# Optimization experiments

Measured on AMD Instinct MI355X. Metric: run time of the kernel, lower is better.

## Reference

```python
import jax, jax.numpy as jnp
import numpy as np

L, H, D, FF = 6, 16, 768, 3072
B, N = 4, 1023
HD = D // H  # 48
EPS = 1e-5


def _layernorm(x, w, b):
    m = jnp.mean(x, axis=-1, keepdims=True)
    v = jnp.mean((x - m) ** 2, axis=-1, keepdims=True)
    return (x - m) / jnp.sqrt(v + EPS) * w + b


def setup_inputs() -> dict:
    key = jax.random.key(0)
    ks = jax.random.split(key, 10)
    ratio = 2.0 ** (-8.0 / H)
    slopes = np.array([ratio ** (i + 1) for i in range(H)], dtype=np.float32)
    return {
        "cls_tokens": jax.random.normal(ks[0], (B, N, D), jnp.float32),
        "cls_token": jax.random.normal(ks[1], (1, 1, D), jnp.float32) * 0.02,
        "log_slopes": jnp.log(jnp.asarray(slopes)),
        "Wqkv": jax.random.normal(ks[2], (L, 3 * D, D), jnp.float32) * 0.02,
        "Wo": jax.random.normal(ks[3], (L, D, D), jnp.float32) * 0.02,
        "Wg": jax.random.normal(ks[4], (L, FF, D), jnp.float32) * 0.02,
        "Wu": jax.random.normal(ks[5], (L, FF, D), jnp.float32) * 0.02,
        "Wd": jax.random.normal(ks[6], (L, D, FF), jnp.float32) * 0.02,
        "ln1_w": jnp.ones((L, D), jnp.float32),
        "ln1_b": jnp.zeros((L, D), jnp.float32),
        "ln2_w": jnp.ones((L, D), jnp.float32),
        "ln2_b": jnp.zeros((L, D), jnp.float32),
        "fin_w": jnp.ones((D,), jnp.float32),
        "fin_b": jnp.zeros((D,), jnp.float32),
    }


def reference(cls_tokens, cls_token, log_slopes, Wqkv, Wo, Wg, Wu, Wd,
              ln1_w, ln1_b, ln2_w, ln2_b, fin_w, fin_b):
    b, n, dmodel = cls_tokens.shape
    S = n + 1
    # learnable ALiBi: -exp(log_slope) * |i - j|, shape (H, S, S)
    pos = jnp.arange(S)
    dist = jnp.abs(pos[None, :] - pos[:, None]).astype(cls_tokens.dtype)
    bias = -(jnp.exp(log_slopes)[:, None, None] * dist[None, :, :])

    x = jnp.concatenate([jnp.broadcast_to(cls_token, (b, 1, dmodel)), cls_tokens], axis=1)
    scale = 1.0 / jnp.sqrt(jnp.asarray(HD, x.dtype))

    for l in range(L):
        h = _layernorm(x, ln1_w[l], ln1_b[l])
        qkv = jnp.einsum('bsd,ed->bse', h, Wqkv[l]).reshape(b, S, 3, H, HD)
        qkv = qkv.transpose(2, 0, 3, 1, 4)  # (3, B, H, S, hd)
        q, k, v = qkv[0], qkv[1], qkv[2]
        scores = jnp.einsum('bhqd,bhkd->bhqk', q, k) * scale + bias[None]
        attn = jax.nn.softmax(scores, axis=-1)
        o = jnp.einsum('bhqk,bhkd->bhqd', attn, v)
        o = o.transpose(0, 2, 1, 3).reshape(b, S, dmodel)
        x = x + jnp.einsum('bsd,ed->bse', o, Wo[l])
        h = _layernorm(x, ln2_w[l], ln2_b[l])
        gate = jax.nn.silu(jnp.einsum('bsd,fd->bsf', h, Wg[l]))
        up = jnp.einsum('bsd,fd->bsf', h, Wu[l])
        x = x + jnp.einsum('bsf,df->bsd', gate * up, Wd[l])

    return _layernorm(x[:, 0, :], fin_w, fin_b)
```

## Files before the change

kernel.cpp:

```cpp
#include <hip/hip_runtime.h>
#include <hip/hip_bf16.h>

#define LNUM 6
#define HNUM 16
#define DMODEL 768
#define FFDIM 3072
#define BATCH 4
#define NTOK 1023
#define SEQ 1024
#define HD 48
#define EPS 1e-5f

typedef __hip_bfloat16 bf16;

__device__ __forceinline__ unsigned short f2bf_raw(float f) {
  bf16 h = __float2bfloat16(f);
  union { bf16 h; unsigned short s; } u; u.h = h; return u.s;
}
__device__ __forceinline__ float bflo(unsigned int u) { return __uint_as_float(u << 16); }
__device__ __forceinline__ float bfhi(unsigned int u) { return __uint_as_float(u & 0xffff0000u); }

__global__ __launch_bounds__(256) void concat_kernel(
    const float* __restrict__ cls_tokens, const float* __restrict__ cls_token,
    float* __restrict__ x) {
  size_t i = (size_t)blockIdx.x * blockDim.x + threadIdx.x;
  const size_t total = (size_t)BATCH * SEQ * DMODEL;
  if (i >= total) return;
  int d = (int)(i % DMODEL);
  size_t bs = i / DMODEL;
  int s = (int)(bs % SEQ);
  int b = (int)(bs / SEQ);
  float v;
  if (s == 0) v = cls_token[d];
  else v = cls_tokens[((size_t)b * NTOK + (s - 1)) * DMODEL + d];
  x[i] = v;
}

#define W_QKV4  442368
#define W_O4    147456
#define W_FF4   589824
__global__ __launch_bounds__(256) void convert_w_kernel(
    const float* __restrict__ wqkv, const float* __restrict__ wo,
    const float* __restrict__ wg, const float* __restrict__ wu,
    const float* __restrict__ wd, bf16* __restrict__ dst) {
  size_t i4 = (size_t)blockIdx.x * 256 + threadIdx.x;
  size_t off4 = i4;
  const float* src;
  if (off4 < W_QKV4) src = wqkv;
  else { off4 -= W_QKV4;
    if (off4 < W_O4) src = wo;
    else { off4 -= W_O4;
      if (off4 < W_FF4) src = wg;
      else { off4 -= W_FF4;
        if (off4 < W_FF4) src = wu;
        else { off4 -= W_FF4; src = wd; } } } }
  float4 v = ((const float4*)src)[off4];
  ushort4 o;
  o.x = f2bf_raw(v.x); o.y = f2bf_raw(v.y);
  o.z = f2bf_raw(v.z); o.w = f2bf_raw(v.w);
  ((ushort4*)dst)[i4] = o;
}

__device__ __forceinline__ void st_ln(float* p, float v) { *p = v; }
__device__ __forceinline__ void st_ln(bf16* p, float v) { *p = __float2bfloat16(v); }

template <typename OUT>
__global__ __launch_bounds__(256) void ln_kernel(
    const float* __restrict__ in, OUT* __restrict__ out,
    const float* __restrict__ w, const float* __restrict__ bias,
    size_t in_stride, size_t out_stride) {
  const int row = blockIdx.x;
  const int tid = threadIdx.x;
  const float* x = in + (size_t)row * in_stride;
  OUT* y = out + (size_t)row * out_stride;

  float v0 = x[tid], v1 = x[tid + 256], v2 = x[tid + 512];
  float s = v0 + v1 + v2;
  float sq = v0 * v0 + v1 * v1 + v2 * v2;

  __shared__ float s_sum[256];
  __shared__ float s_sq[256];
  s_sum[tid] = s;
  s_sq[tid] = sq;
  __syncthreads();
  for (int off = 128; off > 0; off >>= 1) {
    if (tid < off) {
      s_sum[tid] += s_sum[tid + off];
      s_sq[tid] += s_sq[tid + off];
    }
    __syncthreads();
  }
  const float inv_d = 1.0f / (float)DMODEL;
  float mean = s_sum[0] * inv_d;
  float var = s_sq[0] * inv_d - mean * mean;
  float rstd = rsqrtf(var + EPS);

  st_ln(y + tid,       (v0 - mean) * rstd * w[tid]       + bias[tid]);
  st_ln(y + tid + 256, (v1 - mean) * rstd * w[tid + 256] + bias[tid + 256]);
  st_ln(y + tid + 512, (v2 - mean) * rstd * w[tid + 512] + bias[tid + 512]);
}

#define BM 128
#define BN 128
#define BK 32

typedef __attribute__((ext_vector_type(8))) short bfrag;
typedef __attribute__((ext_vector_type(4))) float f32x4;

__device__ __forceinline__ void async_copy16(const void* g, void* l) {
  __builtin_amdgcn_global_load_lds(
      (const __attribute__((address_space(1))) void*)g,
      (__attribute__((address_space(3))) void*)l, 16, 0, 0);
}

template <int CMODE>
__global__ __launch_bounds__(256) void gemm_bf16(
    const bf16* __restrict__ A, const bf16* __restrict__ B,
    void* __restrict__ Cv, int M, int N, int K) {
  __shared__ bf16 As[2][BM][BK];
  __shared__ bf16 Bs[2][BN][BK];

  const int tid = threadIdx.x;
  const int wave = tid >> 6;
  const int lane = tid & 63;
  const int m0 = blockIdx.y * BM;
  const int n0 = blockIdx.x * BN;
  const int wm = (wave & 1) * 64;
  const int wn = (wave >> 1) * 64;

  f32x4 acc[4][4];
#pragma unroll
  for (int i = 0; i < 4; i++)
#pragma unroll
    for (int j = 0; j < 4; j++) acc[i][j] = (f32x4)(0.f);

  const int lrow = lane >> 2;
  const int lcol = (lane & 3) * 8;
  const bf16* Ag[2]; const bf16* Bg[2];
  void *AsB[2][2], *BsB[2][2];
#pragma unroll
  for (int j = 0; j < 2; j++) {
    int c = j * 4 + wave;
    Ag[j] = A + (size_t)(m0 + c * 16 + lrow) * K + lcol;
    Bg[j] = B + (size_t)(n0 + c * 16 + lrow) * K + lcol;
#pragma unroll
    for (int bf = 0; bf < 2; bf++) {
      AsB[bf][j] = (void*)&As[bf][c * 16][0];
      BsB[bf][j] = (void*)&Bs[bf][c * 16][0];
    }
  }

#pragma unroll
  for (int j = 0; j < 2; j++) {
    async_copy16(Ag[j], AsB[0][j]);
    async_copy16(Bg[j], BsB[0][j]);
  }

  const int fr = lane & 15;
  const int fk = (lane >> 4) * 8;
  const int nk = K / BK;

  for (int ki = 0; ki < nk; ki++) {
    const int cur = ki & 1;
    __syncthreads();
    if (ki + 1 < nk) {
      const int k0 = (ki + 1) * BK;
#pragma unroll
      for (int j = 0; j < 2; j++) {
        async_copy16(Ag[j] + k0, AsB[cur ^ 1][j]);
        async_copy16(Bg[j] + k0, BsB[cur ^ 1][j]);
      }
    }
    bfrag a[4], b[4];
#pragma unroll
    for (int i = 0; i < 4; i++) {
      a[i] = *(const bfrag*)&As[cur][wm + i * 16 + fr][fk];
      b[i] = *(const bfrag*)&Bs[cur][wn + i * 16 + fr][fk];
    }
#pragma unroll
    for (int i = 0; i < 4; i++)
#pragma unroll
      for (int j = 0; j < 4; j++)
        acc[i][j] = __builtin_amdgcn_mfma_f32_16x16x32_bf16(a[i], b[j], acc[i][j], 0, 0, 0);
  }

  const int ccol = lane & 15;
  const int crow = (lane >> 4) * 4;
#pragma unroll
  for (int i = 0; i < 4; i++) {
#pragma unroll
    for (int j = 0; j < 4; j++) {
#pragma unroll
      for (int r = 0; r < 4; r++) {
        const size_t gm = m0 + wm + i * 16 + crow + r;
        const size_t gn = n0 + wn + j * 16 + ccol;
        if (CMODE == 2) {
          ((bf16*)Cv)[gm * N + gn] = __float2bfloat16(acc[i][j][r]);
        } else if (CMODE == 1) {
          float* cp = (float*)Cv + gm * N + gn;
          *cp += acc[i][j][r];
        } else {
          ((float*)Cv)[gm * N + gn] = acc[i][j][r];
        }
      }
    }
  }
}

__global__ __launch_bounds__(256) void gemm_gateup(
    const bf16* __restrict__ A, const bf16* __restrict__ Wg,
    const bf16* __restrict__ Wu, bf16* __restrict__ gu, int M, int N, int K) {
  __shared__ bf16 As[2][BM][BK];
  __shared__ bf16 Gs[2][BN][BK];
  __shared__ bf16 Us[2][BN][BK];

  const int tid = threadIdx.x;
  const int wave = tid >> 6;
  const int lane = tid & 63;
  const int m0 = blockIdx.y * BM;
  const int n0 = blockIdx.x * BN;
  const int wm = (wave & 1) * 64;
  const int wn = (wave >> 1) * 64;

  f32x4 accG[4][4], accU[4][4];
#pragma unroll
  for (int i = 0; i < 4; i++)
#pragma unroll
    for (int j = 0; j < 4; j++) { accG[i][j] = (f32x4)(0.f); accU[i][j] = (f32x4)(0.f); }

  const int lrow = lane >> 2;
  const int lcol = (lane & 3) * 8;
  const bf16 *Ag[2], *Gg[2], *Ug[2];
  void *AsB[2][2], *GsB[2][2], *UsB[2][2];
#pragma unroll
  for (int j = 0; j < 2; j++) {
    int c = j * 4 + wave;
    Ag[j] = A + (size_t)(m0 + c * 16 + lrow) * K + lcol;
    Gg[j] = Wg + (size_t)(n0 + c * 16 + lrow) * K + lcol;
    Ug[j] = Wu + (size_t)(n0 + c * 16 + lrow) * K + lcol;
#pragma unroll
    for (int bf = 0; bf < 2; bf++) {
      AsB[bf][j] = (void*)&As[bf][c * 16][0];
      GsB[bf][j] = (void*)&Gs[bf][c * 16][0];
      UsB[bf][j] = (void*)&Us[bf][c * 16][0];
    }
  }

#pragma unroll
  for (int j = 0; j < 2; j++) {
    async_copy16(Ag[j], AsB[0][j]);
    async_copy16(Gg[j], GsB[0][j]);
    async_copy16(Ug[j], UsB[0][j]);
  }

  const int fr = lane & 15;
  const int fk = (lane >> 4) * 8;
  const int nk = K / BK;

  for (int ki = 0; ki < nk; ki++) {
    const int cur = ki & 1;
    __syncthreads();
    if (ki + 1 < nk) {
      const int k0 = (ki + 1) * BK;
#pragma unroll
      for (int j = 0; j < 2; j++) {
        async_copy16(Ag[j] + k0, AsB[cur ^ 1][j]);
        async_copy16(Gg[j] + k0, GsB[cur ^ 1][j]);
        async_copy16(Ug[j] + k0, UsB[cur ^ 1][j]);
      }
    }
    bfrag a[4], g[4], u[4];
#pragma unroll
    for (int i = 0; i < 4; i++) {
      a[i] = *(const bfrag*)&As[cur][wm + i * 16 + fr][fk];
      g[i] = *(const bfrag*)&Gs[cur][wn + i * 16 + fr][fk];
      u[i] = *(const bfrag*)&Us[cur][wn + i * 16 + fr][fk];
    }
#pragma unroll
    for (int i = 0; i < 4; i++)
#pragma unroll
      for (int j = 0; j < 4; j++) {
        accG[i][j] = __builtin_amdgcn_mfma_f32_16x16x32_bf16(a[i], g[j], accG[i][j], 0, 0, 0);
        accU[i][j] = __builtin_amdgcn_mfma_f32_16x16x32_bf16(a[i], u[j], accU[i][j], 0, 0, 0);
      }
  }

  const int ccol = lane & 15;
  const int crow = (lane >> 4) * 4;
#pragma unroll
  for (int i = 0; i < 4; i++) {
#pragma unroll
    for (int j = 0; j < 4; j++) {
#pragma unroll
      for (int r = 0; r < 4; r++) {
        const size_t gm = m0 + wm + i * 16 + crow + r;
        const size_t gn = n0 + wn + j * 16 + ccol;
        const float gv = accG[i][j][r];
        const float uv = accU[i][j][r];
        const float res = gv / (1.0f + __expf(-gv)) * uv;
        gu[gm * N + gn] = __float2bfloat16(res);
      }
    }
  }
}

#define AQT 64
#define AKT 64
#define ASTR 72

__global__ __launch_bounds__(256, 4) void attn_mfma(
    const bf16* __restrict__ qkv, const float* __restrict__ log_slopes,
    bf16* __restrict__ obuf) {
  __shared__ bf16 Qs[AQT][ASTR];
  __shared__ bf16 Ks[AKT][ASTR];
  __shared__ bf16 Vt[HD][ASTR];
  __shared__ bf16 Pt[AQT][ASTR];

  const int tid = threadIdx.x;
  const int wq = tid >> 6;
  const int lane = tid & 63;
  const int l15 = lane & 15;
  const int lh = lane >> 4;
  const int qb = blockIdx.x * AQT;
  const int h = blockIdx.y;
  const int b = blockIdx.z;

  const float scale = 0.14433756729740643f;
  const float slope = __expf(log_slopes[h]);
  const size_t rstride = 3 * DMODEL;
  const bf16* qbase = qkv + ((size_t)(b * SEQ + qb)) * rstride + h * HD;

  for (int it = tid; it < AQT * 2; it += 256) {
    int r = it >> 1, c = it & 1;
    *(uint4*)&Qs[r][48 + c * 8] = make_uint4(0, 0, 0, 0);
    *(uint4*)&Ks[r][48 + c * 8] = make_uint4(0, 0, 0, 0);
  }
  for (int it = tid; it < AQT * 6; it += 256) {
    int r = it / 6, c = it % 6;
    *(uint4*)&Qs[r][c * 8] = *(const uint4*)(qbase + (size_t)r * rstride + c * 8);
  }

  float m[4], l[4];
  f32x4 accO[3];
#pragma unroll
  for (int r = 0; r < 4; r++) { m[r] = -1e30f; l[r] = 0.f; }
#pragma unroll
  for (int t = 0; t < 3; t++) accO[t] = (f32x4)(0.f);

  for (int kb = 0; kb < SEQ; kb += AKT) {
    __syncthreads();
    const bf16* kbase = qkv + ((size_t)(b * SEQ + kb)) * rstride + DMODEL + h * HD;
    for (int it = tid; it < AKT * 6; it += 256) {
      int r = it / 6, c = it % 6;
      *(uint4*)&Ks[r][c * 8] = *(const uint4*)(kbase + (size_t)r * rstride + c * 8);
    }
    if (tid < 192) {
      int p = tid & 31, c = tid >> 5;
      const bf16* v0 = kbase + DMODEL + (size_t)(2 * p) * rstride + c * 8;
      uint4 r0 = *(const uint4*)v0;
      uint4 r1 = *(const uint4*)(v0 + rstride);
      const unsigned int* w0 = (const unsigned int*)&r0;
      const unsigned int* w1 = (const unsigned int*)&r1;
#pragma unroll
      for (int i = 0; i < 8; i++) {
        unsigned int lo = (i & 1) ? (w0[i >> 1] >> 16) : (w0[i >> 1] & 0xffffu);
        unsigned int hi = (i & 1) ? (w1[i >> 1] >> 16) : (w1[i >> 1] & 0xffffu);
        *(unsigned int*)&Vt[c * 8 + i][2 * p] = lo | (hi << 16);
      }
    }
    __syncthreads();

    f32x4 accS[4];
#pragma unroll
    for (int j = 0; j < 4; j++) accS[j] = (f32x4)(0.f);
#pragma unroll
    for (int ks = 0; ks < 2; ks++) {
      bfrag a = *(const bfrag*)&Qs[wq * 16 + l15][ks * 32 + lh * 8];
#pragma unroll
      for (int j = 0; j < 4; j++) {
        bfrag bk = *(const bfrag*)&Ks[j * 16 + l15][ks * 32 + lh * 8];
        accS[j] = __builtin_amdgcn_mfma_f32_16x16x32_bf16(a, bk, accS[j], 0, 0, 0);
      }
    }

    float ps[4][4];
#pragma unroll
    for (int r = 0; r < 4; r++) {
      const int qg = qb + wq * 16 + lh * 4 + r;
      float s[4];
#pragma unroll
      for (int j = 0; j < 4; j++) {
        const int kg = kb + j * 16 + l15;
        s[j] = accS[j][r] * scale - slope * fabsf((float)(qg - kg));
      }
      float mx = fmaxf(fmaxf(s[0], s[1]), fmaxf(s[2], s[3]));
#pragma unroll
      for (int off = 1; off < 16; off <<= 1) mx = fmaxf(mx, __shfl_xor(mx, off, 64));
      const float mnew = fmaxf(m[r], mx);
      const float corr = __expf(m[r] - mnew);
      float rs = 0.f;
#pragma unroll
      for (int j = 0; j < 4; j++) {
        ps[j][r] = __expf(s[j] - mnew);
        rs += ps[j][r];
      }
#pragma unroll
      for (int off = 1; off < 16; off <<= 1) rs += __shfl_xor(rs, off, 64);
      l[r] = l[r] * corr + rs;
      m[r] = mnew;
#pragma unroll
      for (int t = 0; t < 3; t++) accO[t][r] *= corr;
    }

#pragma unroll
    for (int j = 0; j < 4; j++)
#pragma unroll
      for (int r = 0; r < 4; r++)
        Pt[wq * 16 + lh * 4 + r][j * 16 + l15] = __float2bfloat16(ps[j][r]);

#pragma unroll
    for (int ks = 0; ks < 2; ks++) {
      bfrag pa = *(const bfrag*)&Pt[wq * 16 + l15][ks * 32 + lh * 8];
#pragma unroll
      for (int t = 0; t < 3; t++) {
        bfrag vb = *(const bfrag*)&Vt[t * 16 + l15][ks * 32 + lh * 8];
        accO[t] = __builtin_amdgcn_mfma_f32_16x16x32_bf16(pa, vb, accO[t], 0, 0, 0);
      }
    }
  }

#pragma unroll
  for (int r = 0; r < 4; r++) {
    const float inv = 1.0f / l[r];
    bf16* op = obuf + ((size_t)(b * SEQ + qb + wq * 16 + lh * 4 + r)) * DMODEL + h * HD;
#pragma unroll
    for (int t = 0; t < 3; t++)
      op[t * 16 + l15] = __float2bfloat16(accO[t][r] * inv);
  }
}

extern "C" void kernel_launch(void* const* d_in, const int* in_sizes, int n_in,
                              void* d_out, int out_size, void* d_ws, size_t ws_size,
                              hipStream_t stream) {
  const float* cls_tokens = (const float*)d_in[0];
  const float* cls_token  = (const float*)d_in[1];
  const float* log_slopes = (const float*)d_in[2];
  const float* Wqkv = (const float*)d_in[3];
  const float* Wo   = (const float*)d_in[4];
  const float* Wg   = (const float*)d_in[5];
  const float* Wu   = (const float*)d_in[6];
  const float* Wd   = (const float*)d_in[7];
  const float* ln1_w = (const float*)d_in[8];
  const float* ln1_b = (const float*)d_in[9];
  const float* ln2_w = (const float*)d_in[10];
  const float* ln2_b = (const float*)d_in[11];
  const float* fin_w = (const float*)d_in[12];
  const float* fin_b = (const float*)d_in[13];
  float* out = (float*)d_out;

  const size_t ROWS = (size_t)BATCH * SEQ;
  char* wsb = (char*)d_ws;
  float* x    = (float*)(wsb);
  bf16* qkvb  = (bf16*)(wsb + 12582912);
  bf16* hb    = (bf16*)(wsb + 31457280);
  bf16* ob    = (bf16*)(wsb + 37748736);
  bf16* gub   = (bf16*)(wsb + 44040192);
  bf16* wbf   = (bf16*)(wsb + 94371840);

  bf16* wqkv_b = wbf;
  bf16* wo_b   = wbf + 1769472;
  bf16* wg_b   = wbf + 2359296;
  bf16* wu_b   = wbf + 4718592;
  bf16* wd_b   = wbf + 7077888;

  {
    const size_t total = ROWS * DMODEL;
    concat_kernel<<<(int)((total + 255) / 256), 256, 0, stream>>>(cls_tokens, cls_token, x);
  }

  for (int l = 0; l < LNUM; l++) {
    convert_w_kernel<<<9216, 256, 0, stream>>>(
        Wqkv + (size_t)l * 3 * DMODEL * DMODEL, Wo + (size_t)l * DMODEL * DMODEL,
        Wg + (size_t)l * FFDIM * DMODEL, Wu + (size_t)l * FFDIM * DMODEL,
        Wd + (size_t)l * DMODEL * FFDIM, wbf);

    ln_kernel<bf16><<<(int)ROWS, 256, 0, stream>>>(
        x, hb, ln1_w + l * DMODEL, ln1_b + l * DMODEL, DMODEL, DMODEL);
    gemm_bf16<2><<<dim3(3 * DMODEL / BN, ROWS / BM), 256, 0, stream>>>(
        hb, wqkv_b, qkvb, (int)ROWS, 3 * DMODEL, DMODEL);
    attn_mfma<<<dim3(SEQ / AQT, HNUM, BATCH), 256, 0, stream>>>(qkvb, log_slopes, ob);
    gemm_bf16<1><<<dim3(DMODEL / BN, ROWS / BM), 256, 0, stream>>>(
        ob, wo_b, x, (int)ROWS, DMODEL, DMODEL);
    ln_kernel<bf16><<<(int)ROWS, 256, 0, stream>>>(
        x, hb, ln2_w + l * DMODEL, ln2_b + l * DMODEL, DMODEL, DMODEL);
    gemm_gateup<<<dim3(FFDIM / BN, ROWS / BM), 256, 0, stream>>>(
        hb, wg_b, wu_b, gub, (int)ROWS, FFDIM, DMODEL);
    gemm_bf16<1><<<dim3(DMODEL / BN, ROWS / BM), 256, 0, stream>>>(
        gub, wd_b, x, (int)ROWS, DMODEL, FFDIM);
  }

  ln_kernel<float><<<BATCH, 256, 0, stream>>>(x, out, fin_w, fin_b,
                                              (size_t)SEQ * DMODEL, DMODEL);
}
```

Before: 1.886 ms.

## Pre-transpose V, register-prefetch K/V in attention, use narrower N tile for D-output GEMMs

Adds a separate kernel that transposes V into a head-major [d][seq] buffer, so the attention kernel can load K and V tiles with plain vector copies. The next K/V tile is prefetched into registers while the current tile is computed, overlapping global loads with MFMA work. The Wo and down-projection GEMMs now use a 64-wide N tile, doubling the block count to fill more CUs on the 768-wide output. The cost is an extra kernel launch and an extra write and read of V, plus more register pressure in attention.

```diff
diff --git a/kernel.cpp b/kernel.cpp
--- a/kernel.cpp
+++ b/kernel.cpp
@@ -207,6 +207,96 @@
   }
 }
 
+template <int CMODE>
+__global__ __launch_bounds__(256) void gemm_bf16_n64(
+    const bf16* __restrict__ A, const bf16* __restrict__ B,
+    void* __restrict__ Cv, int M, int N, int K) {
+  __shared__ bf16 As[2][BM][BK];
+  __shared__ bf16 Bs[2][64][BK];
+
+  const int tid = threadIdx.x;
+  const int wave = tid >> 6;
+  const int lane = tid & 63;
+  const int m0 = blockIdx.y * BM;
+  const int n0 = blockIdx.x * 64;
+  const int wm = (wave & 1) * 64;
+  const int wn = (wave >> 1) * 32;
+
+  f32x4 acc[4][2];
+#pragma unroll
+  for (int i = 0; i < 4; i++)
+#pragma unroll
+    for (int j = 0; j < 2; j++) acc[i][j] = (f32x4)(0.f);
+
+  const int lrow = lane >> 2;
+  const int lcol = (lane & 3) * 8;
+  const bf16* Ag[2]; const bf16* Bg;
+  void *AsB[2][2], *BsB[2];
+#pragma unroll
+  for (int j = 0; j < 2; j++) {
+    int c = j * 4 + wave;
+    Ag[j] = A + (size_t)(m0 + c * 16 + lrow) * K + lcol;
+#pragma unroll
+    for (int bf = 0; bf < 2; bf++) AsB[bf][j] = (void*)&As[bf][c * 16][0];
+  }
+  Bg = B + (size_t)(n0 + wave * 16 + lrow) * K + lcol;
+#pragma unroll
+  for (int bf = 0; bf < 2; bf++) BsB[bf] = (void*)&Bs[bf][wave * 16][0];
+
+  async_copy16(Ag[0], AsB[0][0]);
+  async_copy16(Ag[1], AsB[0][1]);
+  async_copy16(Bg, BsB[0]);
+
+  const int fr = lane & 15;
+  const int fk = (lane >> 4) * 8;
+  const int nk = K / BK;
+
+  for (int ki = 0; ki < nk; ki++) {
+    const int cur = ki & 1;
+    __syncthreads();
+    if (ki + 1 < nk) {
+      const int k0 = (ki + 1) * BK;
+      async_copy16(Ag[0] + k0, AsB[cur ^ 1][0]);
+      async_copy16(Ag[1] + k0, AsB[cur ^ 1][1]);
+      async_copy16(Bg + k0, BsB[cur ^ 1]);
+    }
+    bfrag a[4], b[2];
+#pragma unroll
+    for (int i = 0; i < 4; i++)
+      a[i] = *(const bfrag*)&As[cur][wm + i * 16 + fr][fk];
+#pragma unroll
+    for (int j = 0; j < 2; j++)
+      b[j] = *(const bfrag*)&Bs[cur][wn + j * 16 + fr][fk];
+#pragma unroll
+    for (int i = 0; i < 4; i++)
+#pragma unroll
+      for (int j = 0; j < 2; j++)
+        acc[i][j] = __builtin_amdgcn_mfma_f32_16x16x32_bf16(a[i], b[j], acc[i][j], 0, 0, 0);
+  }
+
+  const int ccol = lane & 15;
+  const int crow = (lane >> 4) * 4;
+#pragma unroll
+  for (int i = 0; i < 4; i++) {
+#pragma unroll
+    for (int j = 0; j < 2; j++) {
+#pragma unroll
+      for (int r = 0; r < 4; r++) {
+        const size_t gm = m0 + wm + i * 16 + crow + r;
+        const size_t gn = n0 + wn + j * 16 + ccol;
+        if (CMODE == 2) {
+          ((bf16*)Cv)[gm * N + gn] = __float2bfloat16(acc[i][j][r]);
+        } else if (CMODE == 1) {
+          float* cp = (float*)Cv + gm * N + gn;
+          *cp += acc[i][j][r];
+        } else {
+          ((float*)Cv)[gm * N + gn] = acc[i][j][r];
+        }
+      }
+    }
+  }
+}
+
 __global__ __launch_bounds__(256) void gemm_gateup(
     const bf16* __restrict__ A, const bf16* __restrict__ Wg,
     const bf16* __restrict__ Wu, bf16* __restrict__ gu, int M, int N, int K) {
@@ -304,16 +394,48 @@
   }
 }
 
+__global__ __launch_bounds__(256) void transpose_v(
+    const bf16* __restrict__ qkv, bf16* __restrict__ vt) {
+  __shared__ bf16 T[HD][64];
+  const int tid = threadIdx.x;
+  const int kb = blockIdx.x * 64;
+  const int h = blockIdx.y;
+  const int b = blockIdx.z;
+  const size_t rstride = 3 * DMODEL;
+  const bf16* vsrc = qkv + ((size_t)(b * SEQ + kb)) * rstride + 2 * DMODEL + h * HD;
+
+  if (tid < 192) {
+    int p = tid & 31, c = tid >> 5;
+    const bf16* v0 = vsrc + (size_t)(2 * p) * rstride + c * 8;
+    uint4 r0 = *(const uint4*)v0;
+    uint4 r1 = *(const uint4*)(v0 + rstride);
+    const unsigned int* w0 = (const unsigned int*)&r0;
+    const unsigned int* w1 = (const unsigned int*)&r1;
+#pragma unroll
+    for (int i = 0; i < 8; i++) {
+      unsigned int lo = (i & 1) ? (w0[i >> 1] >> 16) : (w0[i >> 1] & 0xffffu);
+      unsigned int hi = (i & 1) ? (w1[i >> 1] >> 16) : (w1[i >> 1] & 0xffffu);
+      *(unsigned int*)&T[c * 8 + i][2 * p] = lo | (hi << 16);
+    }
+  }
+  __syncthreads();
+  for (int it = tid; it < HD * 8; it += 256) {
+    int d = it >> 3, c = it & 7;
+    *(uint4*)(vt + ((size_t)((b * HNUM + h) * HD + d)) * SEQ + kb + c * 8) =
+        *(const uint4*)&T[d][c * 8];
+  }
+}
+
 #define AQT 64
 #define AKT 64
 #define ASTR 72
 
 __global__ __launch_bounds__(256, 4) void attn_mfma(
-    const bf16* __restrict__ qkv, const float* __restrict__ log_slopes,
-    bf16* __restrict__ obuf) {
+    const bf16* __restrict__ qkv, const bf16* __restrict__ vt,
+    const float* __restrict__ log_slopes, bf16* __restrict__ obuf) {
   __shared__ bf16 Qs[AQT][ASTR];
   __shared__ bf16 Ks[AKT][ASTR];
-  __shared__ bf16 Vt[HD][ASTR];
+  __shared__ bf16 Vs[HD][ASTR];
   __shared__ bf16 Pt[AQT][ASTR];
 
   const int tid = threadIdx.x;
@@ -329,6 +451,28 @@
   const float slope = __expf(log_slopes[h]);
   const size_t rstride = 3 * DMODEL;
   const bf16* qbase = qkv + ((size_t)(b * SEQ + qb)) * rstride + h * HD;
+  const bf16* kbase0 = qkv + ((size_t)b * SEQ) * rstride + DMODEL + h * HD;
+  const bf16* vbase0 = vt + ((size_t)((b * HNUM + h) * HD)) * SEQ;
+
+  bf16* ldst[3];
+  size_t goff[3];
+  bool isK[3];
+#pragma unroll
+  for (int j = 0; j < 3; j++) {
+    int id = tid + j * 256;
+    if (id < 384) {
+      int r = id / 6, c = id - r * 6;
+      ldst[j] = &Ks[r][c * 8];
+      goff[j] = (size_t)r * rstride + c * 8;
+      isK[j] = true;
+    } else {
+      id -= 384;
+      int d = id >> 3, c = id & 7;
+      ldst[j] = &Vs[d][c * 8];
+      goff[j] = (size_t)d * SEQ + c * 8;
+      isK[j] = false;
+    }
+  }
 
   for (int it = tid; it < AQT * 2; it += 256) {
     int r = it >> 1, c = it & 1;
@@ -336,9 +480,14 @@
     *(uint4*)&Ks[r][48 + c * 8] = make_uint4(0, 0, 0, 0);
   }
   for (int it = tid; it < AQT * 6; it += 256) {
-    int r = it / 6, c = it % 6;
+    int r = it / 6, c = it - (it / 6) * 6;
     *(uint4*)&Qs[r][c * 8] = *(const uint4*)(qbase + (size_t)r * rstride + c * 8);
   }
+
+  uint4 pre[3];
+#pragma unroll
+  for (int j = 0; j < 3; j++)
+    pre[j] = *(const uint4*)((isK[j] ? kbase0 : vbase0) + goff[j]);
 
   float m[4], l[4];
   f32x4 accO[3];
@@ -349,26 +498,16 @@
 
   for (int kb = 0; kb < SEQ; kb += AKT) {
     __syncthreads();
-    const bf16* kbase = qkv + ((size_t)(b * SEQ + kb)) * rstride + DMODEL + h * HD;
-    for (int it = tid; it < AKT * 6; it += 256) {
-      int r = it / 6, c = it % 6;
-      *(uint4*)&Ks[r][c * 8] = *(const uint4*)(kbase + (size_t)r * rstride + c * 8);
-    }
-    if (tid < 192) {
-      int p = tid & 31, c = tid >> 5;
-      const bf16* v0 = kbase + DMODEL + (size_t)(2 * p) * rstride + c * 8;
-      uint4 r0 = *(const uint4*)v0;
-      uint4 r1 = *(const uint4*)(v0 + rstride);
-      const unsigned int* w0 = (const unsigned int*)&r0;
-      const unsigned int* w1 = (const unsigned int*)&r1;
-#pragma unroll
-      for (int i = 0; i < 8; i++) {
-        unsigned int lo = (i & 1) ? (w0[i >> 1] >> 16) : (w0[i >> 1] & 0xffffu);
-        unsigned int hi = (i & 1) ? (w1[i >> 1] >> 16) : (w1[i >> 1] & 0xffffu);
-        *(unsigned int*)&Vt[c * 8 + i][2 * p] = lo | (hi << 16);
-      }
-    }
+#pragma unroll
+    for (int j = 0; j < 3; j++) *(uint4*)ldst[j] = pre[j];
     __syncthreads();
+    if (kb + AKT < SEQ) {
+      const bf16* kb1 = kbase0 + (size_t)(kb + AKT) * rstride;
+      const bf16* vb1 = vbase0 + (kb + AKT);
+#pragma unroll
+      for (int j = 0; j < 3; j++)
+        pre[j] = *(const uint4*)((isK[j] ? kb1 : vb1) + goff[j]);
+    }
 
     f32x4 accS[4];
 #pragma unroll
@@ -423,7 +562,7 @@
       bfrag pa = *(const bfrag*)&Pt[wq * 16 + l15][ks * 32 + lh * 8];
 #pragma unroll
       for (int t = 0; t < 3; t++) {
-        bfrag vb = *(const bfrag*)&Vt[t * 16 + l15][ks * 32 + lh * 8];
+        bfrag vb = *(const bfrag*)&Vs[t * 16 + l15][ks * 32 + lh * 8];
         accO[t] = __builtin_amdgcn_mfma_f32_16x16x32_bf16(pa, vb, accO[t], 0, 0, 0);
       }
     }
@@ -466,6 +605,7 @@
   bf16* ob    = (bf16*)(wsb + 37748736);
   bf16* gub   = (bf16*)(wsb + 44040192);
   bf16* wbf   = (bf16*)(wsb + 94371840);
+  bf16* vtb   = (bf16*)(wsb + 113246208);
 
   bf16* wqkv_b = wbf;
   bf16* wo_b   = wbf + 1769472;
@@ -488,14 +628,16 @@
         x, hb, ln1_w + l * DMODEL, ln1_b + l * DMODEL, DMODEL, DMODEL);
     gemm_bf16<2><<<dim3(3 * DMODEL / BN, ROWS / BM), 256, 0, stream>>>(
         hb, wqkv_b, qkvb, (int)ROWS, 3 * DMODEL, DMODEL);
-    attn_mfma<<<dim3(SEQ / AQT, HNUM, BATCH), 256, 0, stream>>>(qkvb, log_slopes, ob);
-    gemm_bf16<1><<<dim3(DMODEL / BN, ROWS / BM), 256, 0, stream>>>(
+    transpose_v<<<dim3(SEQ / 64, HNUM, BATCH), 256, 0, stream>>>(qkvb, vtb);
+    attn_mfma<<<dim3(SEQ / AQT, HNUM, BATCH), 256, 0, stream>>>(
+        qkvb, vtb, log_slopes, ob);
+    gemm_bf16_n64<1><<<dim3(DMODEL / 64, ROWS / BM), 256, 0, stream>>>(
         ob, wo_b, x, (int)ROWS, DMODEL, DMODEL);
     ln_kernel<bf16><<<(int)ROWS, 256, 0, stream>>>(
         x, hb, ln2_w + l * DMODEL, ln2_b + l * DMODEL, DMODEL, DMODEL);
     gemm_gateup<<<dim3(FFDIM / BN, ROWS / BM), 256, 0, stream>>>(
         hb, wg_b, wu_b, gub, (int)ROWS, FFDIM, DMODEL);
-    gemm_bf16<1><<<dim3(DMODEL / BN, ROWS / BM), 256, 0, stream>>>(
+    gemm_bf16_n64<1><<<dim3(DMODEL / 64, ROWS / BM), 256, 0, stream>>>(
         gub, wd_b, x, (int)ROWS, DMODEL, FFDIM);
   }
 
```

After: 1.848 ms. -2.0%, faster.
